# Kernel tuning notes

Hardware: AMD Instinct MI355X
Metric: run time of the kernel (lower is better)

The kernel has to match this reference:

```python
import jax, jax.numpy as jnp
import numpy as np

D_MODEL = 1024
NUM_HEADS = 16
D_K = D_MODEL // NUM_HEADS


def setup_inputs() -> dict:
    key = jax.random.key(0)
    ks = jax.random.split(key, 11)
    B, S = 2, 2048
    scale = 1.0 / np.sqrt(D_MODEL)
    inp = {
        "Q": jax.random.normal(ks[0], (B, S, D_MODEL), jnp.float32),
        "K": jax.random.normal(ks[1], (B, S, D_MODEL), jnp.float32),
        "V": jax.random.normal(ks[2], (B, S, D_MODEL), jnp.float32),
        # per-head projection weights stacked on head axis: [H, d_model, d_k]
        "Wq": jax.random.uniform(ks[3], (NUM_HEADS, D_MODEL, D_K), jnp.float32, -scale, scale),
        "bq": jax.random.uniform(ks[4], (NUM_HEADS, D_K), jnp.float32, -scale, scale),
        "Wk": jax.random.uniform(ks[5], (NUM_HEADS, D_MODEL, D_K), jnp.float32, -scale, scale),
        "bk": jax.random.uniform(ks[6], (NUM_HEADS, D_K), jnp.float32, -scale, scale),
        "Wv": jax.random.uniform(ks[7], (NUM_HEADS, D_MODEL, D_K), jnp.float32, -scale, scale),
        "bv": jax.random.uniform(ks[8], (NUM_HEADS, D_K), jnp.float32, -scale, scale),
        "Wo": jax.random.uniform(ks[9], (D_MODEL, D_MODEL), jnp.float32, -scale, scale),
        "bo": jax.random.uniform(ks[10], (D_MODEL,), jnp.float32, -scale, scale),
    }
    return inp


def reference(Q, K, V, Wq, bq, Wk, bk, Wv, bv, Wo, bo):
    # Batched equivalent of the per-head loop: project all heads at once.
    q = jnp.einsum("bsd,hdk->bhsk", Q, Wq) + bq[None, :, None, :]
    k = jnp.einsum("bsd,hdk->bhsk", K, Wk) + bk[None, :, None, :]
    v = jnp.einsum("bsd,hdk->bhsk", V, Wv) + bv[None, :, None, :]
    scores = jnp.einsum("bhqk,bhmk->bhqm", q, k) / jnp.sqrt(jnp.float32(D_K))
    weights = jax.nn.softmax(scores, axis=-1)
    attn = jnp.einsum("bhqm,bhmk->bhqk", weights, v)  # [B,H,S,d_k]
    B, H, S, Dk = attn.shape
    concat = attn.transpose(0, 2, 1, 3).reshape(B, S, H * Dk)  # head-order concat
    return concat @ Wo.T + bo
```

## Files before the change

kernel.cpp:

```cpp
#include <hip/hip_runtime.h>
#include <math.h>

#define BATCH 2
#define SLEN 2048
#define DM 1024
#define NH 16
#define DK 64
#define STILES (SLEN / 64)

typedef __attribute__((ext_vector_type(8))) __bf16 bf16x8;
typedef __attribute__((ext_vector_type(4))) float f32x4;

__device__ __forceinline__ unsigned short f2bf(float x) {
  unsigned u = __builtin_bit_cast(unsigned, x);
  unsigned r = (u + 0x7fffu + ((u >> 16) & 1u)) >> 16;
  return (unsigned short)r;
}
__device__ __forceinline__ float bf2f(unsigned short b) {
  unsigned u = ((unsigned)b) << 16;
  return __builtin_bit_cast(float, u);
}
__device__ __forceinline__ void splitbf(float x, unsigned short& h,
                                        unsigned short& l) {
  unsigned u = __builtin_bit_cast(unsigned, x);
  h = (unsigned short)(u >> 16);
  float hf = __builtin_bit_cast(float, u & 0xffff0000u);
  l = (unsigned short)(__builtin_bit_cast(unsigned, x - hf) >> 16);
}

__device__ __forceinline__ void gld16(const unsigned short* g,
                                      unsigned short* l) {
  __builtin_amdgcn_global_load_lds(
      (const __attribute__((address_space(1))) void*)g,
      (__attribute__((address_space(3))) void*)l, 16, 0, 0);
}

__global__ __launch_bounds__(256)
void convert_w(const float* __restrict__ Wq, const float* __restrict__ Wk,
               const float* __restrict__ Wv, unsigned short* __restrict__ Wqt,
               unsigned short* __restrict__ Wkt,
               unsigned short* __restrict__ Wvt) {
  const int kb = blockIdx.x, h = blockIdx.y, z = blockIdx.z;
  const float* W = (z == 0 ? Wq : z == 1 ? Wk : Wv) +
                   ((size_t)h * DM + kb * 64) * DK;
  unsigned short* D = (z == 0 ? Wqt : z == 1 ? Wkt : Wvt);

  __shared__ float T[64][65];
  const int tid = threadIdx.x;
  {
    int r = tid >> 2, c0 = (tid & 3) * 16;
#pragma unroll
    for (int i = 0; i < 4; ++i) {
      float4 f = *(const float4*)(W + (size_t)r * DK + c0 + i * 4);
      T[r][c0 + i * 4 + 0] = f.x;
      T[r][c0 + i * 4 + 1] = f.y;
      T[r][c0 + i * 4 + 2] = f.z;
      T[r][c0 + i * 4 + 3] = f.w;
    }
  }
  __syncthreads();
  int j = tid >> 2, p = tid & 3;
  int n = h * 64 + j;
  int kloc = p * 16;
  unsigned short hi[16], lo[16];
#pragma unroll
  for (int i = 0; i < 16; ++i) splitbf(T[kloc + i][j], hi[i], lo[i]);
  int kglob = kb * 64 + kloc;
  int blk = kglob >> 5;
  int c0 = (kglob & 31) >> 3;
  int key = n & 7;
  unsigned short* rowp = D + (size_t)n * 2048 + blk * 64;
  uint4 u0, u1;
  u0.x = (unsigned)hi[0] | ((unsigned)hi[1] << 16);
  u0.y = (unsigned)hi[2] | ((unsigned)hi[3] << 16);
  u0.z = (unsigned)hi[4] | ((unsigned)hi[5] << 16);
  u0.w = (unsigned)hi[6] | ((unsigned)hi[7] << 16);
  u1.x = (unsigned)hi[8] | ((unsigned)hi[9] << 16);
  u1.y = (unsigned)hi[10] | ((unsigned)hi[11] << 16);
  u1.z = (unsigned)hi[12] | ((unsigned)hi[13] << 16);
  u1.w = (unsigned)hi[14] | ((unsigned)hi[15] << 16);
  *(uint4*)(rowp + ((c0 ^ key)) * 8) = u0;
  *(uint4*)(rowp + (((c0 + 1) ^ key)) * 8) = u1;
  u0.x = (unsigned)lo[0] | ((unsigned)lo[1] << 16);
  u0.y = (unsigned)lo[2] | ((unsigned)lo[3] << 16);
  u0.z = (unsigned)lo[4] | ((unsigned)lo[5] << 16);
  u0.w = (unsigned)lo[6] | ((unsigned)lo[7] << 16);
  u1.x = (unsigned)lo[8] | ((unsigned)lo[9] << 16);
  u1.y = (unsigned)lo[10] | ((unsigned)lo[11] << 16);
  u1.z = (unsigned)lo[12] | ((unsigned)lo[13] << 16);
  u1.w = (unsigned)lo[14] | ((unsigned)lo[15] << 16);
  *(uint4*)(rowp + (((c0 + 4) ^ key)) * 8) = u0;
  *(uint4*)(rowp + (((c0 + 5) ^ key)) * 8) = u1;
}

__global__ __launch_bounds__(256)
void proj_gemm(const float* __restrict__ Qin, const float* __restrict__ Kin,
               const float* __restrict__ Vin,
               const unsigned short* __restrict__ Wqt,
               const unsigned short* __restrict__ Wkt,
               const unsigned short* __restrict__ Wvt,
               const float* __restrict__ bq, const float* __restrict__ bk,
               const float* __restrict__ bv, unsigned short* __restrict__ q_all,
               unsigned short* __restrict__ k_all,
               unsigned short* __restrict__ vt) {
  const int ntile = blockIdx.x, mt = blockIdx.y, z = blockIdx.z;
  const float* A = (z == 0 ? Qin : z == 1 ? Kin : Vin);
  const unsigned short* B = (z == 0 ? Wqt : z == 1 ? Wkt : Wvt);
  const float* bias = (z == 0 ? bq : z == 1 ? bk : bv);

  __shared__ alignas(16) unsigned short As[128 * 64];
  __shared__ alignas(16) unsigned short Bs[2][128 * 64];

  const int tid = threadIdx.x;
  const int lane = tid & 63, w = tid >> 6;
  const int l15 = lane & 15, quad = lane >> 4;
  const int wm = (w & 1) * 64, wn = (w >> 1) * 64;
  const int kx = l15 & 7;

  const float* Ap = A + (size_t)(mt * 128) * DM;
  const unsigned short* Bp = B + (size_t)(ntile * 128) * 2048;

  float4 areg[4];
#pragma unroll
  for (int it = 0; it < 4; ++it) {
    int c = tid + it * 256;
    int r = c >> 3, seg = c & 7;
    areg[it] = *(const float4*)(Ap + (size_t)r * DM + seg * 4);
  }
#pragma unroll
  for (int it = 0; it < 4; ++it) {
    int s = tid + it * 256;
    int r = s >> 3, seg = s & 7;
    gld16(Bp + (size_t)r * 2048 + seg * 8, &Bs[0][s * 8]);
  }

  f32x4 acc[4][4];
#pragma unroll
  for (int i = 0; i < 4; ++i)
#pragma unroll
    for (int j = 0; j < 4; ++j) acc[i][j] = (f32x4){0.f, 0.f, 0.f, 0.f};

  int cur = 0;
  for (int kk = 0; kk < 32; ++kk) {
#pragma unroll
    for (int it = 0; it < 4; ++it) {
      int c = tid + it * 256;
      int r = c >> 3, seg = c & 7;
      int key = r & 7, ch = seg >> 1, off = (seg & 1) * 4;
      ushort4 h4, l4;
      splitbf(areg[it].x, h4.x, l4.x);
      splitbf(areg[it].y, h4.y, l4.y);
      splitbf(areg[it].z, h4.z, l4.z);
      splitbf(areg[it].w, h4.w, l4.w);
      *(ushort4*)&As[r * 64 + ((ch ^ key)) * 8 + off] = h4;
      *(ushort4*)&As[r * 64 + (((ch + 4) ^ key)) * 8 + off] = l4;
    }
    __syncthreads();

    if (kk + 1 < 32) {
      int k0n = (kk + 1) * 32;
#pragma unroll
      for (int it = 0; it < 4; ++it) {
        int c = tid + it * 256;
        int r = c >> 3, seg = c & 7;
        areg[it] = *(const float4*)(Ap + (size_t)r * DM + k0n + seg * 4);
      }
#pragma unroll
      for (int it = 0; it < 4; ++it) {
        int s = tid + it * 256;
        int r = s >> 3, seg = s & 7;
        gld16(Bp + (size_t)r * 2048 + (k0n >> 5) * 64 + seg * 8,
              &Bs[cur ^ 1][s * 8]);
      }
    }

    bf16x8 ah[4], al[4];
#pragma unroll
    for (int i = 0; i < 4; ++i) {
      const unsigned short* p = &As[(wm + i * 16 + l15) * 64];
      ah[i] = *(const bf16x8*)(p + ((quad ^ kx)) * 8);
      al[i] = *(const bf16x8*)(p + (((quad + 4) ^ kx)) * 8);
    }
#pragma unroll
    for (int j = 0; j < 4; ++j) {
      const unsigned short* p = &Bs[cur][(wn + j * 16 + l15) * 64];
      bf16x8 bh = *(const bf16x8*)(p + ((quad ^ kx)) * 8);
      bf16x8 bl = *(const bf16x8*)(p + (((quad + 4) ^ kx)) * 8);
#pragma unroll
      for (int i = 0; i < 4; ++i) {
        acc[i][j] = __builtin_amdgcn_mfma_f32_16x16x32_bf16(ah[i], bh, acc[i][j], 0, 0, 0);
        acc[i][j] = __builtin_amdgcn_mfma_f32_16x16x32_bf16(al[i], bh, acc[i][j], 0, 0, 0);
        acc[i][j] = __builtin_amdgcn_mfma_f32_16x16x32_bf16(ah[i], bl, acc[i][j], 0, 0, 0);
      }
    }
    __syncthreads();
    cur ^= 1;
  }

  if (z <= 1) {
    unsigned short* dst = (z == 0 ? q_all : k_all);
#pragma unroll
    for (int i = 0; i < 4; ++i)
#pragma unroll
      for (int j = 0; j < 4; ++j) {
        int n = ntile * 128 + wn + j * 16 + l15;
        int hh_ = n >> 6, d = n & 63;
        int chi = (d >> 5) * 8 + ((d & 31) >> 3);
        float bn = bias[n];
#pragma unroll
        for (int r = 0; r < 4; ++r) {
          int m = mt * 128 + wm + i * 16 + quad * 4 + r;
          int key = m & 15;
          size_t rb = (size_t)m * 2048 + hh_ * 128;
          unsigned short hv, lv;
          splitbf(acc[i][j][r] + bn, hv, lv);
          dst[rb + ((chi ^ key)) * 8 + (d & 7)] = hv;
          dst[rb + (((chi + 4) ^ key)) * 8 + (d & 7)] = lv;
        }
      }
  } else {
#pragma unroll
    for (int i = 0; i < 4; ++i)
#pragma unroll
      for (int j = 0; j < 4; ++j) {
        int n = ntile * 128 + wn + j * 16 + l15;
        int h = n >> 6, d = n & 63;
        float bn = bias[n];
        int m0 = mt * 128 + wm + i * 16 + quad * 4;
        int b = m0 >> 11, s0_ = m0 & 2047;
        int kt = s0_ >> 6, sl = s0_ & 63;
        int ch = sl >> 3, off = sl & 7, key = d & 15;
        ushort4 h4, l4;
        splitbf(acc[i][j][0] + bn, h4.x, l4.x);
        splitbf(acc[i][j][1] + bn, h4.y, l4.y);
        splitbf(acc[i][j][2] + bn, h4.z, l4.z);
        splitbf(acc[i][j][3] + bn, h4.w, l4.w);
        size_t base =
            (size_t)(b * NH + h) * 262144 + (size_t)d * 4096 + kt * 128;
        *(ushort4*)(vt + base + ((ch ^ key)) * 8 + off) = h4;
        *(ushort4*)(vt + base + (((ch + 8) ^ key)) * 8 + off) = l4;
      }
  }
}

__global__ __launch_bounds__(256)
void out_gemm(const unsigned short* __restrict__ a_all,
              const float* __restrict__ Wo, const float* __restrict__ bo,
              float* __restrict__ out) {
  const int ntile = blockIdx.x, mt = blockIdx.y;

  __shared__ alignas(16) unsigned short As[2][128 * 64];
  __shared__ alignas(16) unsigned short Bs[128 * 64];

  const int tid = threadIdx.x;
  const int lane = tid & 63, w = tid >> 6;
  const int l15 = lane & 15, quad = lane >> 4;
  const int wm = (w & 1) * 64, wn = (w >> 1) * 64;
  const int kx = l15 & 7;

  const unsigned short* Ap = a_all + (size_t)(mt * 128) * 2048;
  const float* Bp = Wo + (size_t)(ntile * 128) * DM;

  float4 breg[4];
#pragma unroll
  for (int it = 0; it < 4; ++it) {
    int c = tid + it * 256;
    int r = c >> 3, seg = c & 7;
    breg[it] = *(const float4*)(Bp + (size_t)r * DM + seg * 4);
  }
#pragma unroll
  for (int it = 0; it < 4; ++it) {
    int s = tid + it * 256;
    int r = s >> 3, seg = s & 7;
    gld16(Ap + (size_t)r * 2048 + seg * 8, &As[0][s * 8]);
  }

  f32x4 acc[4][4];
#pragma unroll
  for (int i = 0; i < 4; ++i)
#pragma unroll
    for (int j = 0; j < 4; ++j) acc[i][j] = (f32x4){0.f, 0.f, 0.f, 0.f};

  int cur = 0;
  for (int kk = 0; kk < 32; ++kk) {
#pragma unroll
    for (int it = 0; it < 4; ++it) {
      int c = tid + it * 256;
      int r = c >> 3, seg = c & 7;
      int key = r & 7, ch = seg >> 1, off = (seg & 1) * 4;
      ushort4 h4, l4;
      splitbf(breg[it].x, h4.x, l4.x);
      splitbf(breg[it].y, h4.y, l4.y);
      splitbf(breg[it].z, h4.z, l4.z);
      splitbf(breg[it].w, h4.w, l4.w);
      *(ushort4*)&Bs[r * 64 + ((ch ^ key)) * 8 + off] = h4;
      *(ushort4*)&Bs[r * 64 + (((ch + 4) ^ key)) * 8 + off] = l4;
    }
    __syncthreads();

    if (kk + 1 < 32) {
      int k0n = (kk + 1) * 32;
#pragma unroll
      for (int it = 0; it < 4; ++it) {
        int c = tid + it * 256;
        int r = c >> 3, seg = c & 7;
        breg[it] = *(const float4*)(Bp + (size_t)r * DM + k0n + seg * 4);
      }
#pragma unroll
      for (int it = 0; it < 4; ++it) {
        int s = tid + it * 256;
        int r = s >> 3, seg = s & 7;
        gld16(Ap + (size_t)r * 2048 + (k0n >> 5) * 64 + seg * 8,
              &As[cur ^ 1][s * 8]);
      }
    }

    bf16x8 ah[4], al[4];
#pragma unroll
    for (int i = 0; i < 4; ++i) {
      const unsigned short* p = &As[cur][(wm + i * 16 + l15) * 64];
      ah[i] = *(const bf16x8*)(p + ((quad ^ kx)) * 8);
      al[i] = *(const bf16x8*)(p + (((quad + 4) ^ kx)) * 8);
    }
#pragma unroll
    for (int j = 0; j < 4; ++j) {
      const unsigned short* p = &Bs[(wn + j * 16 + l15) * 64];
      bf16x8 bh = *(const bf16x8*)(p + ((quad ^ kx)) * 8);
      bf16x8 bl = *(const bf16x8*)(p + (((quad + 4) ^ kx)) * 8);
#pragma unroll
      for (int i = 0; i < 4; ++i) {
        acc[i][j] = __builtin_amdgcn_mfma_f32_16x16x32_bf16(ah[i], bh, acc[i][j], 0, 0, 0);
        acc[i][j] = __builtin_amdgcn_mfma_f32_16x16x32_bf16(al[i], bh, acc[i][j], 0, 0, 0);
        acc[i][j] = __builtin_amdgcn_mfma_f32_16x16x32_bf16(ah[i], bl, acc[i][j], 0, 0, 0);
      }
    }
    __syncthreads();
    cur ^= 1;
  }

#pragma unroll
  for (int i = 0; i < 4; ++i)
#pragma unroll
    for (int j = 0; j < 4; ++j) {
      int n = ntile * 128 + wn + j * 16 + l15;
      float bn = bo[n];
#pragma unroll
      for (int r = 0; r < 4; ++r) {
        int m = mt * 128 + wm + i * 16 + quad * 4 + r;
        out[(size_t)m * DM + n] = acc[i][j][r] + bn;
      }
    }
}

__global__ __launch_bounds__(256)
void attn_kernel(const unsigned short* __restrict__ q_all,
                 const unsigned short* __restrict__ k_all,
                 const unsigned short* __restrict__ vt,
                 unsigned short* __restrict__ a_all) {
  const int qt = blockIdx.x, h = blockIdx.y, b = blockIdx.z;
  const unsigned short* vp = vt + (size_t)(b * NH + h) * 262144;

  __shared__ alignas(16) unsigned short Ks[64 * 128];
  __shared__ alignas(16) unsigned short Vs[64 * 128];
  __shared__ alignas(16) unsigned short Ps[128 * 64];

  const int tid = threadIdx.x;
  const int lane = tid & 63;
  const int w = tid >> 6;
  const int l15 = lane & 15;
  const int quad = lane >> 4;

  bf16x8 qf[2][2][2];
#pragma unroll
  for (int rt = 0; rt < 2; ++rt) {
    const unsigned short* qrow =
        q_all + (size_t)(b * SLEN + qt * 128 + w * 32 + rt * 16 + l15) * 2048 +
        h * 128;
#pragma unroll
    for (int kb = 0; kb < 2; ++kb) {
      qf[rt][kb][0] = *(const bf16x8*)(qrow + ((kb * 8 + quad) ^ l15) * 8);
      qf[rt][kb][1] = *(const bf16x8*)(qrow + ((kb * 8 + quad + 4) ^ l15) * 8);
    }
  }

  f32x4 o[2][4];
  float lpart[2][4];
#pragma unroll
  for (int rt = 0; rt < 2; ++rt)
#pragma unroll
    for (int nt = 0; nt < 4; ++nt) {
      o[rt][nt] = (f32x4){0.f, 0.f, 0.f, 0.f};
      lpart[rt][nt] = 0.f;
    }

  for (int kt = 0; kt < STILES; ++kt) {
    const unsigned short* ksrc =
        k_all + (size_t)(b * SLEN + kt * 64) * 2048 + h * 128;
#pragma unroll
    for (int it = 0; it < 4; ++it) {
      int ss = it * 256 + tid;
      int r = ss >> 4, p = ss & 15;
      gld16(ksrc + (size_t)r * 2048 + p * 8, &Ks[ss * 8]);
    }
#pragma unroll
    for (int it = 0; it < 4; ++it) {
      int ss = it * 256 + tid;
      int d = ss >> 4, p = ss & 15;
      gld16(vp + (size_t)d * 4096 + kt * 128 + p * 8, &Vs[ss * 8]);
    }
    __syncthreads();

    f32x4 sc[2][4];
#pragma unroll
    for (int rt = 0; rt < 2; ++rt)
#pragma unroll
      for (int ct = 0; ct < 4; ++ct) sc[rt][ct] = (f32x4){0.f, 0.f, 0.f, 0.f};
#pragma unroll
    for (int ct = 0; ct < 4; ++ct) {
      const unsigned short* kbase = &Ks[(ct * 16 + l15) * 128];
#pragma unroll
      for (int kb = 0; kb < 2; ++kb) {
        bf16x8 kh = *(const bf16x8*)(kbase + ((kb * 8 + quad) ^ l15) * 8);
        bf16x8 kl = *(const bf16x8*)(kbase + ((kb * 8 + quad + 4) ^ l15) * 8);
#pragma unroll
        for (int rt = 0; rt < 2; ++rt) {
          sc[rt][ct] = __builtin_amdgcn_mfma_f32_16x16x32_bf16(qf[rt][kb][0], kh, sc[rt][ct], 0, 0, 0);
          sc[rt][ct] = __builtin_amdgcn_mfma_f32_16x16x32_bf16(qf[rt][kb][0], kl, sc[rt][ct], 0, 0, 0);
          sc[rt][ct] = __builtin_amdgcn_mfma_f32_16x16x32_bf16(qf[rt][kb][1], kh, sc[rt][ct], 0, 0, 0);
        }
      }
    }

#pragma unroll
    for (int rt = 0; rt < 2; ++rt)
#pragma unroll
      for (int ct = 0; ct < 4; ++ct)
#pragma unroll
        for (int r = 0; r < 4; ++r) {
          float e = __expf(sc[rt][ct][r] * 0.125f);
          lpart[rt][r] += e;
          int prow = w * 32 + rt * 16 + quad * 4 + r;
          int pkey = (prow >> 1) & 7;
          Ps[prow * 64 + (((ct * 2 + (l15 >> 3)) ^ pkey)) * 8 + (l15 & 7)] =
              f2bf(e);
        }
    __syncthreads();

    int rk = (l15 >> 1) & 7;
#pragma unroll
    for (int kb = 0; kb < 2; ++kb) {
      bf16x8 pf[2];
#pragma unroll
      for (int rt = 0; rt < 2; ++rt)
        pf[rt] = *(const bf16x8*)(&Ps[(w * 32 + rt * 16 + l15) * 64 +
                                      (((kb * 4 + quad) ^ rk)) * 8]);
#pragma unroll
      for (int nt = 0; nt < 4; ++nt) {
        const unsigned short* vb = &Vs[(nt * 16 + l15) * 128];
        bf16x8 vh = *(const bf16x8*)(vb + (((kb * 4 + quad) ^ l15)) * 8);
        bf16x8 vl = *(const bf16x8*)(vb + (((kb * 4 + quad + 8) ^ l15)) * 8);
#pragma unroll
        for (int rt = 0; rt < 2; ++rt) {
          o[rt][nt] = __builtin_amdgcn_mfma_f32_16x16x32_bf16(pf[rt], vh, o[rt][nt], 0, 0, 0);
          o[rt][nt] = __builtin_amdgcn_mfma_f32_16x16x32_bf16(pf[rt], vl, o[rt][nt], 0, 0, 0);
        }
      }
    }
    __syncthreads();
  }

#pragma unroll
  for (int rt = 0; rt < 2; ++rt) {
    float inv[4];
#pragma unroll
    for (int r = 0; r < 4; ++r) {
      float lv = lpart[rt][r];
#pragma unroll
      for (int m = 1; m < 16; m <<= 1) lv += __shfl_xor(lv, m, 64);
      inv[r] = 1.f / lv;
    }
#pragma unroll
    for (int nt = 0; nt < 4; ++nt) {
      int c = h * 64 + nt * 16 + l15;
      int Bb = c >> 5;
      int d32 = c & 31;
      int ch = d32 >> 3, off = d32 & 7;
#pragma unroll
      for (int r = 0; r < 4; ++r) {
        float val = o[rt][nt][r] * inv[r];
        int srow = qt * 128 + w * 32 + rt * 16 + quad * 4 + r;
        int key = srow & 7;
        size_t g = (size_t)(b * SLEN + srow) * 2048 + Bb * 64;
        unsigned short hv, lv2;
        splitbf(val, hv, lv2);
        a_all[g + ((ch ^ key)) * 8 + off] = hv;
        a_all[g + (((ch + 4) ^ key)) * 8 + off] = lv2;
      }
    }
  }
}

extern "C" void kernel_launch(void* const* d_in, const int* in_sizes, int n_in,
                              void* d_out, int out_size, void* d_ws,
                              size_t ws_size, hipStream_t stream) {
  (void)in_sizes; (void)n_in; (void)out_size; (void)ws_size;
  const float* Q = (const float*)d_in[0];
  const float* K = (const float*)d_in[1];
  const float* V = (const float*)d_in[2];
  const float* Wq = (const float*)d_in[3];
  const float* bq = (const float*)d_in[4];
  const float* Wk = (const float*)d_in[5];
  const float* bk = (const float*)d_in[6];
  const float* Wv = (const float*)d_in[7];
  const float* bv = (const float*)d_in[8];
  const float* Wo = (const float*)d_in[9];
  const float* bo = (const float*)d_in[10];
  float* out = (float*)d_out;

  unsigned short* us = (unsigned short*)d_ws;
  const size_t M8 = 8u * 1024 * 1024;
  unsigned short* q_all = us;
  unsigned short* k_all = us + M8;
  unsigned short* vt = us + 2 * M8;
  unsigned short* a_all = us + 3 * M8;
  unsigned short* Wqt = a_all;
  unsigned short* Wkt = a_all + 2 * 1024 * 1024;
  unsigned short* Wvt = a_all + 4 * 1024 * 1024;

  convert_w<<<dim3(16, 16, 3), 256, 0, stream>>>(Wq, Wk, Wv, Wqt, Wkt, Wvt);
  proj_gemm<<<dim3(8, 32, 3), 256, 0, stream>>>(Q, K, V, Wqt, Wkt, Wvt, bq,
                                                bk, bv, q_all, k_all, vt);
  attn_kernel<<<dim3(SLEN / 128, NH, BATCH), 256, 0, stream>>>(q_all, k_all,
                                                               vt, a_all);
  out_gemm<<<dim3(8, 32), 256, 0, stream>>>(a_all, Wo, bo, out);
}
```

Measured before the change: 388.6 us.

## Pre-split Wo to bf16 pairs, shrink out_gemm tiles, double-buffer proj A tile

Adds a convert_wo kernel that splits Wo into swizzled hi/lo bf16 once, so out_gemm can load both operands with async gld16 double buffering instead of converting fp32 in its main loop. The out_gemm tile drops to 64x128 with a doubled grid for better occupancy and CU coverage. proj_gemm gets a double-buffered A tile and loses one __syncthreads per iteration. The changes add an extra launch, reuse the q_all buffer as scratch for Wot, and cut per-block data reuse in out_gemm.

```diff
diff --git a/kernel.cpp b/kernel.cpp
--- a/kernel.cpp
+++ b/kernel.cpp
@@ -94,6 +94,23 @@
 }
 
 __global__ __launch_bounds__(256)
+void convert_wo(const float* __restrict__ Wo, unsigned short* __restrict__ Wot) {
+  const int n = blockIdx.x;
+  const int t = threadIdx.x;
+  const int k0 = t * 4;
+  float4 f = *(const float4*)(Wo + (size_t)n * DM + k0);
+  ushort4 h4, l4;
+  splitbf(f.x, h4.x, l4.x);
+  splitbf(f.y, h4.y, l4.y);
+  splitbf(f.z, h4.z, l4.z);
+  splitbf(f.w, h4.w, l4.w);
+  int blk = k0 >> 5, ch = (k0 & 31) >> 3, off = k0 & 7, key = n & 7;
+  unsigned short* rowp = Wot + (size_t)n * 2048 + blk * 64;
+  *(ushort4*)(rowp + ((ch ^ key)) * 8 + off) = h4;
+  *(ushort4*)(rowp + (((ch + 4) ^ key)) * 8 + off) = l4;
+}
+
+__global__ __launch_bounds__(256)
 void proj_gemm(const float* __restrict__ Qin, const float* __restrict__ Kin,
                const float* __restrict__ Vin,
                const unsigned short* __restrict__ Wqt,
@@ -108,7 +125,7 @@
   const unsigned short* B = (z == 0 ? Wqt : z == 1 ? Wkt : Wvt);
   const float* bias = (z == 0 ? bq : z == 1 ? bk : bv);
 
-  __shared__ alignas(16) unsigned short As[128 * 64];
+  __shared__ alignas(16) unsigned short As[2][128 * 64];
   __shared__ alignas(16) unsigned short Bs[2][128 * 64];
 
   const int tid = threadIdx.x;
@@ -152,8 +169,8 @@
       splitbf(areg[it].y, h4.y, l4.y);
       splitbf(areg[it].z, h4.z, l4.z);
       splitbf(areg[it].w, h4.w, l4.w);
-      *(ushort4*)&As[r * 64 + ((ch ^ key)) * 8 + off] = h4;
-      *(ushort4*)&As[r * 64 + (((ch + 4) ^ key)) * 8 + off] = l4;
+      *(ushort4*)&As[cur][r * 64 + ((ch ^ key)) * 8 + off] = h4;
+      *(ushort4*)&As[cur][r * 64 + (((ch + 4) ^ key)) * 8 + off] = l4;
     }
     __syncthreads();
 
@@ -177,7 +194,7 @@
     bf16x8 ah[4], al[4];
 #pragma unroll
     for (int i = 0; i < 4; ++i) {
-      const unsigned short* p = &As[(wm + i * 16 + l15) * 64];
+      const unsigned short* p = &As[cur][(wm + i * 16 + l15) * 64];
       ah[i] = *(const bf16x8*)(p + ((quad ^ kx)) * 8);
       al[i] = *(const bf16x8*)(p + (((quad + 4) ^ kx)) * 8);
     }
@@ -193,7 +210,6 @@
         acc[i][j] = __builtin_amdgcn_mfma_f32_16x16x32_bf16(ah[i], bl, acc[i][j], 0, 0, 0);
       }
     }
-    __syncthreads();
     cur ^= 1;
   }
 
@@ -245,86 +261,71 @@
 
 __global__ __launch_bounds__(256)
 void out_gemm(const unsigned short* __restrict__ a_all,
-              const float* __restrict__ Wo, const float* __restrict__ bo,
-              float* __restrict__ out) {
+              const unsigned short* __restrict__ Wot,
+              const float* __restrict__ bo, float* __restrict__ out) {
   const int ntile = blockIdx.x, mt = blockIdx.y;
 
-  __shared__ alignas(16) unsigned short As[2][128 * 64];
-  __shared__ alignas(16) unsigned short Bs[128 * 64];
+  __shared__ alignas(16) unsigned short As[2][64 * 64];
+  __shared__ alignas(16) unsigned short Bs[2][128 * 64];
 
   const int tid = threadIdx.x;
   const int lane = tid & 63, w = tid >> 6;
   const int l15 = lane & 15, quad = lane >> 4;
-  const int wm = (w & 1) * 64, wn = (w >> 1) * 64;
+  const int wn = w * 32;
   const int kx = l15 & 7;
 
-  const unsigned short* Ap = a_all + (size_t)(mt * 128) * 2048;
-  const float* Bp = Wo + (size_t)(ntile * 128) * DM;
-
-  float4 breg[4];
-#pragma unroll
-  for (int it = 0; it < 4; ++it) {
-    int c = tid + it * 256;
-    int r = c >> 3, seg = c & 7;
-    breg[it] = *(const float4*)(Bp + (size_t)r * DM + seg * 4);
+  const unsigned short* Ap = a_all + (size_t)(mt * 64) * 2048;
+  const unsigned short* Bp = Wot + (size_t)(ntile * 128) * 2048;
+
+#pragma unroll
+  for (int it = 0; it < 2; ++it) {
+    int s = tid + it * 256;
+    int r = s >> 3, seg = s & 7;
+    gld16(Ap + (size_t)r * 2048 + seg * 8, &As[0][s * 8]);
   }
 #pragma unroll
   for (int it = 0; it < 4; ++it) {
     int s = tid + it * 256;
     int r = s >> 3, seg = s & 7;
-    gld16(Ap + (size_t)r * 2048 + seg * 8, &As[0][s * 8]);
-  }
-
-  f32x4 acc[4][4];
+    gld16(Bp + (size_t)r * 2048 + seg * 8, &Bs[0][s * 8]);
+  }
+
+  f32x4 acc[4][2];
 #pragma unroll
   for (int i = 0; i < 4; ++i)
 #pragma unroll
-    for (int j = 0; j < 4; ++j) acc[i][j] = (f32x4){0.f, 0.f, 0.f, 0.f};
+    for (int j = 0; j < 2; ++j) acc[i][j] = (f32x4){0.f, 0.f, 0.f, 0.f};
 
   int cur = 0;
   for (int kk = 0; kk < 32; ++kk) {
-#pragma unroll
-    for (int it = 0; it < 4; ++it) {
-      int c = tid + it * 256;
-      int r = c >> 3, seg = c & 7;
-      int key = r & 7, ch = seg >> 1, off = (seg & 1) * 4;
-      ushort4 h4, l4;
-      splitbf(breg[it].x, h4.x, l4.x);
-      splitbf(breg[it].y, h4.y, l4.y);
-      splitbf(breg[it].z, h4.z, l4.z);
-      splitbf(breg[it].w, h4.w, l4.w);
-      *(ushort4*)&Bs[r * 64 + ((ch ^ key)) * 8 + off] = h4;
-      *(ushort4*)&Bs[r * 64 + (((ch + 4) ^ key)) * 8 + off] = l4;
-    }
     __syncthreads();
 
     if (kk + 1 < 32) {
-      int k0n = (kk + 1) * 32;
-#pragma unroll
-      for (int it = 0; it < 4; ++it) {
-        int c = tid + it * 256;
-        int r = c >> 3, seg = c & 7;
-        breg[it] = *(const float4*)(Bp + (size_t)r * DM + k0n + seg * 4);
+      int blk = ((kk + 1)) * 64;
+#pragma unroll
+      for (int it = 0; it < 2; ++it) {
+        int s = tid + it * 256;
+        int r = s >> 3, seg = s & 7;
+        gld16(Ap + (size_t)r * 2048 + blk + seg * 8, &As[cur ^ 1][s * 8]);
       }
 #pragma unroll
       for (int it = 0; it < 4; ++it) {
         int s = tid + it * 256;
         int r = s >> 3, seg = s & 7;
-        gld16(Ap + (size_t)r * 2048 + (k0n >> 5) * 64 + seg * 8,
-              &As[cur ^ 1][s * 8]);
+        gld16(Bp + (size_t)r * 2048 + blk + seg * 8, &Bs[cur ^ 1][s * 8]);
       }
     }
 
     bf16x8 ah[4], al[4];
 #pragma unroll
     for (int i = 0; i < 4; ++i) {
-      const unsigned short* p = &As[cur][(wm + i * 16 + l15) * 64];
+      const unsigned short* p = &As[cur][(i * 16 + l15) * 64];
       ah[i] = *(const bf16x8*)(p + ((quad ^ kx)) * 8);
       al[i] = *(const bf16x8*)(p + (((quad + 4) ^ kx)) * 8);
     }
 #pragma unroll
-    for (int j = 0; j < 4; ++j) {
-      const unsigned short* p = &Bs[(wn + j * 16 + l15) * 64];
+    for (int j = 0; j < 2; ++j) {
+      const unsigned short* p = &Bs[cur][(wn + j * 16 + l15) * 64];
       bf16x8 bh = *(const bf16x8*)(p + ((quad ^ kx)) * 8);
       bf16x8 bl = *(const bf16x8*)(p + (((quad + 4) ^ kx)) * 8);
 #pragma unroll
@@ -334,19 +335,18 @@
         acc[i][j] = __builtin_amdgcn_mfma_f32_16x16x32_bf16(ah[i], bl, acc[i][j], 0, 0, 0);
       }
     }
-    __syncthreads();
     cur ^= 1;
   }
 
 #pragma unroll
   for (int i = 0; i < 4; ++i)
 #pragma unroll
-    for (int j = 0; j < 4; ++j) {
+    for (int j = 0; j < 2; ++j) {
       int n = ntile * 128 + wn + j * 16 + l15;
       float bn = bo[n];
 #pragma unroll
       for (int r = 0; r < 4; ++r) {
-        int m = mt * 128 + wm + i * 16 + quad * 4 + r;
+        int m = mt * 64 + i * 16 + quad * 4 + r;
         out[(size_t)m * DM + n] = acc[i][j][r] + bn;
       }
     }
@@ -526,11 +526,13 @@
   unsigned short* Wqt = a_all;
   unsigned short* Wkt = a_all + 2 * 1024 * 1024;
   unsigned short* Wvt = a_all + 4 * 1024 * 1024;
+  unsigned short* Wot = q_all;
 
   convert_w<<<dim3(16, 16, 3), 256, 0, stream>>>(Wq, Wk, Wv, Wqt, Wkt, Wvt);
   proj_gemm<<<dim3(8, 32, 3), 256, 0, stream>>>(Q, K, V, Wqt, Wkt, Wvt, bq,
                                                 bk, bv, q_all, k_all, vt);
   attn_kernel<<<dim3(SLEN / 128, NH, BATCH), 256, 0, stream>>>(q_all, k_all,
                                                                vt, a_all);
-  out_gemm<<<dim3(8, 32), 256, 0, stream>>>(a_all, Wo, bo, out);
-}
+  convert_wo<<<dim3(1024), 256, 0, stream>>>(Wo, Wot);
+  out_gemm<<<dim3(8, 64), 256, 0, stream>>>(a_all, Wot, bo, out);
+}
```

After: 371.1 us. -4.5%, faster.
